# Performance work log

Measured on AMD Instinct MI355X. Metric: run time of the kernel, lower is better.

## Reference

```python
import jax, jax.numpy as jnp
import numpy as np

B, S, E, D, DE = 8, 128, 50, 300, 50  # batch, seq, edge_dim, gcn_dim, dep_embed_dim
EPS = 1e-6


def setup_inputs() -> dict:
    key = jax.random.key(0)
    ks = jax.random.split(key, 9)
    weight_prob_softmax = jax.nn.softmax(jax.random.normal(ks[0], (B, S, S, E)), axis=2)
    weight_adj = jax.random.normal(ks[1], (B, S, S, E))
    gcn_inputs = jax.random.normal(ks[2], (B, S, D))
    # self-loop added to adjacency after permute -> [B, E, S, S]; identity loops
    self_loop = jnp.broadcast_to(jnp.eye(S, dtype=jnp.float32), (B, E, S, S))
    W_w = jax.random.normal(ks[3], (D, D)) * 0.05          # gcn linear (in, out)
    W_b = jnp.zeros((D,))
    ln_a = jnp.ones((D,))
    ln_b = jnp.zeros((D,))
    refine_W = jax.random.normal(ks[4], (2 * D + 3 * E, DE)) * 0.05  # (750, 50)
    refine_b = jnp.zeros((DE,))
    return {
        "weight_prob_softmax": weight_prob_softmax,
        "weight_adj": weight_adj,
        "gcn_inputs": gcn_inputs,
        "self_loop": self_loop,
        "W_w": W_w, "W_b": W_b,
        "ln_a": ln_a, "ln_b": ln_b,
        "refine_W": refine_W, "refine_b": refine_b,
    }


def reference(weight_prob_softmax, weight_adj, gcn_inputs, self_loop,
              W_w, W_b, ln_a, ln_b, refine_W, refine_b):
    b, s, d = gcn_inputs.shape
    e = weight_prob_softmax.shape[-1]
    # [B,S,S,E] -> [B,E,S,S], add self loops
    wps = jnp.transpose(weight_prob_softmax, (0, 3, 1, 2)) + self_loop
    # per-relation-channel message passing: Ax[b,e,i,:] = sum_j wps[b,e,i,j] * x[b,j,:]
    Ax = jnp.einsum('beij,bjd->beid', wps, gcn_inputs)
    Ax = Ax.mean(axis=1)  # avg pooling over edge channels -> [B,S,D]
    h = Ax @ W_w + W_b
    # LayerNorm with unbiased std (torch x.std default) and (std + eps)
    mean = h.mean(axis=-1, keepdims=True)
    var_unbiased = jnp.sum((h - mean) ** 2, axis=-1, keepdims=True) / (d - 1)
    std = jnp.sqrt(var_unbiased)
    h = ln_a * (h - mean) / (std + EPS) + ln_b
    node = jax.nn.relu(h)  # [B,S,D]
    # node1[b,i,j] = node[b,j]; node2[b,i,j] = node[b,i]
    node1 = jnp.broadcast_to(node[:, None, :, :], (b, s, s, d))
    node2 = jnp.broadcast_to(node[:, :, None, :], (b, s, s, d))
    # diagonal edge features: [B,E,S] -> [B,S,E]
    diag = jnp.transpose(jnp.diagonal(weight_adj, axis1=1, axis2=2), (0, 2, 1))
    edge_i = jnp.broadcast_to(diag[:, None, :, :], (b, s, s, e))  # edge_i[b,i,j]=diag[b,j]
    edge_j = jnp.broadcast_to(diag[:, :, None, :], (b, s, s, e))  # edge_j[b,i,j]=diag[b,i]
    feat = jnp.concatenate([weight_adj, edge_i, edge_j, node1, node2], axis=-1)
    edge_out = feat @ refine_W + refine_b  # [B,S,S,DE]
    return node, edge_out
```

## Files before the change

### kernel.cpp

```cpp
#include <hip/hip_runtime.h>
#include <hip/hip_bf16.h>


typedef __bf16 bf16x8 __attribute__((ext_vector_type(8)));
typedef float f32x4 __attribute__((ext_vector_type(4)));

__device__ __forceinline__ unsigned short f2bf(float f) {
    __hip_bfloat16 h = __float2bfloat16(f);
    union { __hip_bfloat16 h; unsigned short u; } c; c.h = h; return c.u;
}

__global__ void __launch_bounds__(320) k_xw(
    const float* __restrict__ x, const float* __restrict__ Ww,
    float* __restrict__ XW)
{
    __shared__ __align__(16) float xr[304];
    int tid = threadIdx.x;
    int row = blockIdx.x;
    if (tid < 300) xr[tid] = x[(size_t)row * 300 + tid];
    else if (tid < 304) xr[tid] = 0.f;
    __syncthreads();
    if (tid < 300) {
        const float* wp = Ww + tid;
        const f32x4* x4 = (const f32x4*)xr;
        float acc = 0.f;
#pragma unroll 5
        for (int k4 = 0; k4 < 75; ++k4) {
            f32x4 xv = x4[k4];
            int k = k4 * 4;
            acc += xv[0] * wp[(k + 0) * 300];
            acc += xv[1] * wp[(k + 1) * 300];
            acc += xv[2] * wp[(k + 2) * 300];
            acc += xv[3] * wp[(k + 3) * 300];
        }
        XW[(size_t)row * 300 + tid] = acc;
    }
}

__global__ void __launch_bounds__(512) k_node(
    const float* __restrict__ wps,
    const float* __restrict__ wa,
    const float* __restrict__ XW,
    const float* __restrict__ Wb,
    const float* __restrict__ lna,
    const float* __restrict__ lnb,
    const float* __restrict__ Rw,
    const float* __restrict__ rb,
    float* __restrict__ node_out,
    float* __restrict__ R1, float* __restrict__ R2)
{
    __shared__ __align__(16) float Ml[128][4];
    __shared__ float hl[4][304];
    __shared__ float nodeL[4][304];
    __shared__ float diag[4][52];
    __shared__ float stats[8];
    __shared__ float part1[14][200];
    __shared__ float part2[14][200];
    int tid = threadIdx.x;
    int b = blockIdx.x >> 5;
    int ig = blockIdx.x & 31;
    int row0 = b * 128 + ig * 4;

    if (tid < 200) {
        int r = tid / 50, e = tid % 50;
        diag[r][e] = wa[(((size_t)(row0 + r)) * 128 + (ig * 4 + r)) * 50 + e];
    }
    {
        int r = tid >> 7, j = tid & 127;
        const float2* p = (const float2*)(wps + ((size_t)(row0 + r)) * 6400 + j * 50);
        float s = 0.f;
#pragma unroll
        for (int n = 0; n < 25; ++n) { float2 v = p[n]; s += v.x + v.y; }
        Ml[j][r] = s * (1.0f / 50.0f) + (((ig * 4 + r) == j) ? 1.0f : 0.0f);
    }
    __syncthreads();

    if (tid < 300) {
        float wb = Wb[tid];
        float h0 = wb, h1 = wb, h2 = wb, h3 = wb;
        const float* xwp = XW + (size_t)b * 38400 + tid;
        const f32x4* M4 = (const f32x4*)Ml;
#pragma unroll 16
        for (int j = 0; j < 128; ++j) {
            float xv = xwp[j * 300];
            f32x4 m = M4[j];
            h0 += m[0] * xv; h1 += m[1] * xv; h2 += m[2] * xv; h3 += m[3] * xv;
        }
        hl[0][tid] = h0; hl[1][tid] = h1; hl[2][tid] = h2; hl[3][tid] = h3;
    } else if (tid >= 312) {
        int t = tid - 312, p = t / 50, k = t % 50;
        int e0 = p * 13, e1 = (e0 + 13 < 50) ? e0 + 13 : 50;
        float r1a[4] = {0.f, 0.f, 0.f, 0.f};
        float r2a[4] = {0.f, 0.f, 0.f, 0.f};
        for (int e = e0; e < e1; ++e) {
            float w1 = Rw[(50 + e) * 50 + k];
            float w2 = Rw[(100 + e) * 50 + k];
#pragma unroll
            for (int r = 0; r < 4; ++r) {
                r1a[r] += diag[r][e] * w1;
                r2a[r] += diag[r][e] * w2;
            }
        }
#pragma unroll
        for (int r = 0; r < 4; ++r) {
            part1[p][r * 50 + k] = r1a[r];
            part2[p][r * 50 + k] = r2a[r];
        }
    }
    __syncthreads();

    if (tid < 256) {
        int wv = tid >> 6, lane = tid & 63;
        float s1 = 0.f, s2 = 0.f;
        for (int dd = lane; dd < 300; dd += 64) {
            float v = hl[wv][dd]; s1 += v; s2 += v * v;
        }
        for (int off = 32; off > 0; off >>= 1) {
            s1 += __shfl_down(s1, off);
            s2 += __shfl_down(s2, off);
        }
        if (lane == 0) {
            float mean = s1 * (1.0f / 300.0f);
            float var = (s2 - 300.0f * mean * mean) * (1.0f / 299.0f);
            var = fmaxf(var, 0.0f);
            stats[wv * 2] = mean;
            stats[wv * 2 + 1] = 1.0f / (sqrtf(var) + 1e-6f);
        }
    }
    __syncthreads();

    if (tid < 300) {
        float la = lna[tid], lb = lnb[tid];
#pragma unroll
        for (int r = 0; r < 4; ++r) {
            float v = la * (hl[r][tid] - stats[r * 2]) * stats[r * 2 + 1] + lb;
            v = fmaxf(v, 0.0f);
            node_out[(size_t)(row0 + r) * 300 + tid] = v;
            nodeL[r][tid] = v;
        }
    }
    __syncthreads();

    if (tid < 500) {
        int p = tid / 50, k = tid % 50;
        int d0 = p * 30;
        float r1a[4] = {0.f, 0.f, 0.f, 0.f};
        float r2a[4] = {0.f, 0.f, 0.f, 0.f};
#pragma unroll 6
        for (int d = d0; d < d0 + 30; ++d) {
            float w1 = Rw[(150 + d) * 50 + k];
            float w2 = Rw[(450 + d) * 50 + k];
#pragma unroll
            for (int r = 0; r < 4; ++r) {
                r1a[r] += nodeL[r][d] * w1;
                r2a[r] += nodeL[r][d] * w2;
            }
        }
#pragma unroll
        for (int r = 0; r < 4; ++r) {
            part1[4 + p][r * 50 + k] = r1a[r];
            part2[4 + p][r * 50 + k] = r2a[r];
        }
    }
    __syncthreads();

    if (tid < 200) {
        int r = tid / 50, k = tid % 50;
        float s1 = 0.f, s2 = rb[k];
#pragma unroll
        for (int p = 0; p < 14; ++p) {
            s1 += part1[p][r * 50 + k];
            s2 += part2[p][r * 50 + k];
        }
        R1[(size_t)(row0 + r) * 50 + k] = s1;
        R2[(size_t)(row0 + r) * 50 + k] = s2;
    }
}

__global__ void __launch_bounds__(256) k_edge(
    const float* __restrict__ wa,
    const float* __restrict__ Rw,
    const float* __restrict__ R1, const float* __restrict__ R2,
    float* __restrict__ eout)
{
    __shared__ __align__(16) unsigned char smem[27648];
    unsigned short* waA  = (unsigned short*)smem;
    unsigned short* rwBT = (unsigned short*)(smem + 18432);
    float* outF = (float*)smem;
    int tid = threadIdx.x;
    int bi = blockIdx.x;
    int b = bi >> 7;

    for (int idx = tid; idx < 2304; idx += 256) ((unsigned int*)rwBT)[idx] = 0u;
    for (int idx = tid; idx < 1408; idx += 256) {
        int j = idx / 11, c = idx % 11;
        *((unsigned int*)(waA + j * 72 + 50) + c) = 0u;
    }
    __syncthreads();

    const float2* wap = (const float2*)(wa + (size_t)bi * 6400);
    for (int idx = tid; idx < 3200; idx += 256) {
        float2 v = wap[idx];
        int f = idx * 2;
        int j = f / 50, e = f % 50;
        unsigned int pack = (unsigned int)f2bf(v.x) | ((unsigned int)f2bf(v.y) << 16);
        *(unsigned int*)(waA + j * 72 + e) = pack;
    }
    for (int idx = tid; idx < 2500; idx += 256) {
        int e = idx / 50, kk = idx % 50;
        rwBT[kk * 72 + e] = f2bf(Rw[idx]);
    }
    __syncthreads();

    int lane = tid & 63, wv = tid >> 6;
    int q = lane >> 4, lr = lane & 15;
    f32x4 acc[2][4] = {};

#pragma unroll
    for (int ks = 0; ks < 2; ++ks) {
        int e0 = ks * 32 + q * 8;
        bf16x8 a0 = *(const bf16x8*)&waA[(wv * 32 + lr) * 72 + e0];
        bf16x8 a1 = *(const bf16x8*)&waA[(wv * 32 + 16 + lr) * 72 + e0];
#pragma unroll
        for (int nt = 0; nt < 4; ++nt) {
            bf16x8 bb = *(const bf16x8*)&rwBT[(nt * 16 + lr) * 72 + e0];
            acc[0][nt] = __builtin_amdgcn_mfma_f32_16x16x32_bf16(a0, bb, acc[0][nt], 0, 0, 0);
            acc[1][nt] = __builtin_amdgcn_mfma_f32_16x16x32_bf16(a1, bb, acc[1][nt], 0, 0, 0);
        }
    }
    __syncthreads();

    const float* r2p = R2 + (size_t)bi * 50;
#pragma unroll
    for (int nt = 0; nt < 4; ++nt) {
        int kk = nt * 16 + lr;
        if (kk < 50) {
            float r2v = r2p[kk];
#pragma unroll
            for (int mi = 0; mi < 2; ++mi) {
                int jbase = wv * 32 + mi * 16 + q * 4;
#pragma unroll
                for (int r = 0; r < 4; ++r)
                    outF[(jbase + r) * 50 + kk] = acc[mi][nt][r] + r2v;
            }
        }
    }
    __syncthreads();

    const float4* R1b = (const float4*)(R1 + (size_t)b * 6400);
    const float4* L4  = (const float4*)outF;
    float4* op4 = (float4*)(eout + (size_t)bi * 6400);
    for (int f4 = tid; f4 < 1600; f4 += 256) {
        float4 v = L4[f4];
        float4 r = R1b[f4];
        v.x += r.x; v.y += r.y; v.z += r.z; v.w += r.w;
        op4[f4] = v;
    }
}

extern "C" void kernel_launch(void* const* d_in, const int* in_sizes, int n_in,
                              void* d_out, int out_size, void* d_ws, size_t ws_size,
                              hipStream_t stream)
{
    const float* wps = (const float*)d_in[0];
    const float* wa  = (const float*)d_in[1];
    const float* x   = (const float*)d_in[2];
    const float* Ww  = (const float*)d_in[4];
    const float* Wb  = (const float*)d_in[5];
    const float* lna = (const float*)d_in[6];
    const float* lnb = (const float*)d_in[7];
    const float* Rw  = (const float*)d_in[8];
    const float* rb  = (const float*)d_in[9];

    float* R1 = (float*)d_ws;
    float* R2 = ((float*)d_ws) + 51200;

    float* node_out = (float*)d_out;
    float* edge_out = node_out + 307200;
    float* XW = edge_out;

    k_xw  <<<1024, 320, 0, stream>>>(x, Ww, XW);
    k_node<<<256, 512, 0, stream>>>(wps, wa, XW, Wb, lna, lnb, Rw, rb,
                                    node_out, R1, R2);
    k_edge<<<1024, 256, 0, stream>>>(wa, Rw, R1, R2, edge_out);
}
```

Baseline: 160.3 us.

## Restructure k_node to one row per block with coalesced staged loads

k_node now runs one output row per 256-thread block over 1024 blocks, replacing four rows per 512-thread block over 256 blocks. The row of weight_prob_softmax is staged into shared memory with coalesced float4 loads before the per-neighbour edge-channel sums. The LayerNorm reduction and the refine projections are reorganised to match. This raises parallelism and load coalescing, but XW and Rw are now reread once per row instead of once per four rows.

```diff
diff --git a/kernel.cpp b/kernel.cpp
--- a/kernel.cpp
+++ b/kernel.cpp
@@ -37,7 +37,7 @@
     }
 }
 
-__global__ void __launch_bounds__(512) k_node(
+__global__ void __launch_bounds__(256) k_node(
     const float* __restrict__ wps,
     const float* __restrict__ wa,
     const float* __restrict__ XW,
@@ -49,131 +49,108 @@
     float* __restrict__ node_out,
     float* __restrict__ R1, float* __restrict__ R2)
 {
-    __shared__ __align__(16) float Ml[128][4];
-    __shared__ float hl[4][304];
-    __shared__ float nodeL[4][304];
-    __shared__ float diag[4][52];
-    __shared__ float stats[8];
-    __shared__ float part1[14][200];
-    __shared__ float part2[14][200];
+    __shared__ __align__(16) float stage[6400];
+    __shared__ float Ml[128];
+    __shared__ float srcL[352];
+    __shared__ float p1s[5][50], p2s[5][50];
+    __shared__ float red[8];
+    __shared__ float stats[2];
     int tid = threadIdx.x;
-    int b = blockIdx.x >> 5;
-    int ig = blockIdx.x & 31;
-    int row0 = b * 128 + ig * 4;
-
-    if (tid < 200) {
-        int r = tid / 50, e = tid % 50;
-        diag[r][e] = wa[(((size_t)(row0 + r)) * 128 + (ig * 4 + r)) * 50 + e];
-    }
+    int row = blockIdx.x;
+    int b = row >> 7, i = row & 127;
+
+    const float4* w4 = (const float4*)(wps + (size_t)row * 6400);
+    float4* s4 = (float4*)stage;
+    for (int t = tid; t < 1600; t += 256) s4[t] = w4[t];
+    if (tid < 50) srcL[tid] = wa[((size_t)row * 128 + i) * 50 + tid];
+    if (tid >= 350 - 256 && tid < 96) {}
+    __syncthreads();
+
+    if (tid < 128) {
+        const float* p = stage + tid * 50;
+        float s = 0.f;
+#pragma unroll
+        for (int e = 0; e < 50; ++e) s += p[e];
+        Ml[tid] = s * (1.0f / 50.0f) + ((tid == i) ? 1.0f : 0.0f);
+    }
+    __syncthreads();
+
+    int d0 = tid;
+    bool has2 = (tid < 44);
+    int d1 = has2 ? 256 + tid : 299;
+    float h0 = Wb[d0];
+    float h1 = Wb[d1];
     {
-        int r = tid >> 7, j = tid & 127;
-        const float2* p = (const float2*)(wps + ((size_t)(row0 + r)) * 6400 + j * 50);
-        float s = 0.f;
-#pragma unroll
-        for (int n = 0; n < 25; ++n) { float2 v = p[n]; s += v.x + v.y; }
-        Ml[j][r] = s * (1.0f / 50.0f) + (((ig * 4 + r) == j) ? 1.0f : 0.0f);
-    }
-    __syncthreads();
-
-    if (tid < 300) {
-        float wb = Wb[tid];
-        float h0 = wb, h1 = wb, h2 = wb, h3 = wb;
-        const float* xwp = XW + (size_t)b * 38400 + tid;
-        const f32x4* M4 = (const f32x4*)Ml;
+        const float* xp = XW + (size_t)b * 38400;
 #pragma unroll 16
         for (int j = 0; j < 128; ++j) {
-            float xv = xwp[j * 300];
-            f32x4 m = M4[j];
-            h0 += m[0] * xv; h1 += m[1] * xv; h2 += m[2] * xv; h3 += m[3] * xv;
-        }
-        hl[0][tid] = h0; hl[1][tid] = h1; hl[2][tid] = h2; hl[3][tid] = h3;
-    } else if (tid >= 312) {
-        int t = tid - 312, p = t / 50, k = t % 50;
-        int e0 = p * 13, e1 = (e0 + 13 < 50) ? e0 + 13 : 50;
-        float r1a[4] = {0.f, 0.f, 0.f, 0.f};
-        float r2a[4] = {0.f, 0.f, 0.f, 0.f};
-        for (int e = e0; e < e1; ++e) {
-            float w1 = Rw[(50 + e) * 50 + k];
-            float w2 = Rw[(100 + e) * 50 + k];
-#pragma unroll
-            for (int r = 0; r < 4; ++r) {
-                r1a[r] += diag[r][e] * w1;
-                r2a[r] += diag[r][e] * w2;
-            }
-        }
-#pragma unroll
-        for (int r = 0; r < 4; ++r) {
-            part1[p][r * 50 + k] = r1a[r];
-            part2[p][r * 50 + k] = r2a[r];
-        }
-    }
-    __syncthreads();
-
-    if (tid < 256) {
-        int wv = tid >> 6, lane = tid & 63;
-        float s1 = 0.f, s2 = 0.f;
-        for (int dd = lane; dd < 300; dd += 64) {
-            float v = hl[wv][dd]; s1 += v; s2 += v * v;
-        }
+            float m = Ml[j];
+            h0 += m * xp[j * 300 + d0];
+            h1 += m * xp[j * 300 + d1];
+        }
+    }
+
+    {
+        float s1 = h0 + (has2 ? h1 : 0.f);
+        float s2 = h0 * h0 + (has2 ? h1 * h1 : 0.f);
         for (int off = 32; off > 0; off >>= 1) {
             s1 += __shfl_down(s1, off);
             s2 += __shfl_down(s2, off);
         }
-        if (lane == 0) {
-            float mean = s1 * (1.0f / 300.0f);
-            float var = (s2 - 300.0f * mean * mean) * (1.0f / 299.0f);
-            var = fmaxf(var, 0.0f);
-            stats[wv * 2] = mean;
-            stats[wv * 2 + 1] = 1.0f / (sqrtf(var) + 1e-6f);
-        }
-    }
-    __syncthreads();
-
-    if (tid < 300) {
-        float la = lna[tid], lb = lnb[tid];
-#pragma unroll
-        for (int r = 0; r < 4; ++r) {
-            float v = la * (hl[r][tid] - stats[r * 2]) * stats[r * 2 + 1] + lb;
-            v = fmaxf(v, 0.0f);
-            node_out[(size_t)(row0 + r) * 300 + tid] = v;
-            nodeL[r][tid] = v;
-        }
-    }
-    __syncthreads();
-
-    if (tid < 500) {
+        int wv = tid >> 6, lane = tid & 63;
+        if (lane == 0) { red[wv] = s1; red[4 + wv] = s2; }
+    }
+    __syncthreads();
+    if (tid == 0) {
+        float s1 = red[0] + red[1] + red[2] + red[3];
+        float s2 = red[4] + red[5] + red[6] + red[7];
+        float mean = s1 * (1.0f / 300.0f);
+        float var = (s2 - 300.0f * mean * mean) * (1.0f / 299.0f);
+        var = fmaxf(var, 0.0f);
+        stats[0] = mean;
+        stats[1] = 1.0f / (sqrtf(var) + 1e-6f);
+    }
+    __syncthreads();
+
+    {
+        float mean = stats[0], inv = stats[1];
+        float n0 = fmaxf(lna[d0] * (h0 - mean) * inv + lnb[d0], 0.f);
+        node_out[(size_t)row * 300 + d0] = n0;
+        srcL[50 + d0] = n0;
+        if (has2) {
+            float n1 = fmaxf(lna[d1] * (h1 - mean) * inv + lnb[d1], 0.f);
+            node_out[(size_t)row * 300 + d1] = n1;
+            srcL[50 + d1] = n1;
+        }
+    }
+    __syncthreads();
+
+    if (tid < 250) {
         int p = tid / 50, k = tid % 50;
-        int d0 = p * 30;
-        float r1a[4] = {0.f, 0.f, 0.f, 0.f};
-        float r2a[4] = {0.f, 0.f, 0.f, 0.f};
-#pragma unroll 6
-        for (int d = d0; d < d0 + 30; ++d) {
-            float w1 = Rw[(150 + d) * 50 + k];
-            float w2 = Rw[(450 + d) * 50 + k];
-#pragma unroll
-            for (int r = 0; r < 4; ++r) {
-                r1a[r] += nodeL[r][d] * w1;
-                r2a[r] += nodeL[r][d] * w2;
-            }
-        }
-#pragma unroll
-        for (int r = 0; r < 4; ++r) {
-            part1[4 + p][r * 50 + k] = r1a[r];
-            part2[4 + p][r * 50 + k] = r2a[r];
-        }
-    }
-    __syncthreads();
-
-    if (tid < 200) {
-        int r = tid / 50, k = tid % 50;
-        float s1 = 0.f, s2 = rb[k];
-#pragma unroll
-        for (int p = 0; p < 14; ++p) {
-            s1 += part1[p][r * 50 + k];
-            s2 += part2[p][r * 50 + k];
-        }
-        R1[(size_t)(row0 + r) * 50 + k] = s1;
-        R2[(size_t)(row0 + r) * 50 + k] = s2;
+        int srcOff, w1b, w2b, len;
+        if (p == 0) { srcOff = 0;  w1b = 50 * 50;  w2b = 100 * 50; len = 50; }
+        else {
+            int dd = (p - 1) * 75;
+            srcOff = 50 + dd; w1b = (150 + dd) * 50; w2b = (450 + dd) * 50; len = 75;
+        }
+        float r1 = 0.f, r2 = 0.f;
+        const float* w1p = Rw + w1b + k;
+        const float* w2p = Rw + w2b + k;
+#pragma unroll 5
+        for (int t = 0; t < len; ++t) {
+            float sv = srcL[srcOff + t];
+            r1 += sv * w1p[t * 50];
+            r2 += sv * w2p[t * 50];
+        }
+        p1s[p][k] = r1; p2s[p][k] = r2;
+    }
+    __syncthreads();
+    if (tid < 50) {
+        float s1 = 0.f, s2 = rb[tid];
+#pragma unroll
+        for (int p = 0; p < 5; ++p) { s1 += p1s[p][tid]; s2 += p2s[p][tid]; }
+        R1[(size_t)row * 50 + tid] = s1;
+        R2[(size_t)row * 50 + tid] = s2;
     }
 }
 
@@ -280,7 +257,7 @@
     float* XW = edge_out;
 
     k_xw  <<<1024, 320, 0, stream>>>(x, Ww, XW);
-    k_node<<<256, 512, 0, stream>>>(wps, wa, XW, Wb, lna, lnb, Rw, rb,
-                                    node_out, R1, R2);
+    k_node<<<1024, 256, 0, stream>>>(wps, wa, XW, Wb, lna, lnb, Rw, rb,
+                                     node_out, R1, R2);
     k_edge<<<1024, 256, 0, stream>>>(wa, Rw, R1, R2, edge_out);
 }
```

Result: slower. 166.5 us (+3.9%).
